# Optimization experiments

Hardware: AMD Instinct MI355X
Metric: run time of the kernel (lower is better)

Reference implementation:

```python
import jax, jax.numpy as jnp
import numpy as np

B, S, D = 2, 2048, 1024
H, KH = 16, 4            # query heads, kv heads
DK = D // H              # 64
REP = H // KH            # queries per kv head


def _rope(x):
    # x: (B, h, S, dk); non-interleaved rotate-half RoPE as in source
    dk = x.shape[-1]
    half = dk // 2
    seq = x.shape[2]
    theta = 10000.0 ** (-(jnp.arange(half, dtype=jnp.float32) / half))
    pos = jnp.arange(seq, dtype=jnp.float32)
    freqs = pos[:, None] * theta[None, :]          # (S, half)
    cos = jnp.cos(freqs)[None, None]               # (1,1,S,half)
    sin = jnp.sin(freqs)[None, None]
    x1, x2 = x[..., :half], x[..., half:]
    return jnp.concatenate([x1 * cos - x2 * sin, x2 * cos + x1 * sin], axis=-1)


def setup_inputs() -> dict:
    key = jax.random.key(0)
    ks = jax.random.split(key, 9)
    sd = 1.0 / np.sqrt(D)
    x = jax.random.normal(ks[0], (B, S, D), dtype=jnp.float32)
    # causal mask: 1 where attend allowed, 0 where masked (mask==0 -> -inf)
    mask = jnp.tril(jnp.ones((S, S), dtype=jnp.int32))[None, None]
    Wq = jax.random.normal(ks[1], (D, H * DK), dtype=jnp.float32) * sd
    bq = jnp.zeros((H * DK,), dtype=jnp.float32)
    Wk = jax.random.normal(ks[2], (D, KH * DK), dtype=jnp.float32) * sd
    bk = jnp.zeros((KH * DK,), dtype=jnp.float32)
    Wv = jax.random.normal(ks[3], (D, KH * DK), dtype=jnp.float32) * sd
    bv = jnp.zeros((KH * DK,), dtype=jnp.float32)
    Wo = jax.random.normal(ks[4], (H * DK, D), dtype=jnp.float32) * sd
    bo = jnp.zeros((D,), dtype=jnp.float32)
    return {"x": x, "mask": mask, "Wq": Wq, "bq": bq, "Wk": Wk, "bk": bk,
            "Wv": Wv, "bv": bv, "Wo": Wo, "bo": bo}


def reference(x, mask, Wq, bq, Wk, bk, Wv, bv, Wo, bo):
    b, s, _ = x.shape
    q = (x @ Wq + bq).reshape(b, s, H, DK).transpose(0, 2, 1, 3)   # (B,H,S,DK)
    k = (x @ Wk + bk).reshape(b, s, KH, DK).transpose(0, 2, 1, 3)  # (B,KH,S,DK)
    v = (x @ Wv + bv).reshape(b, s, KH, DK).transpose(0, 2, 1, 3)
    q = _rope(q)
    k = _rope(k)
    k = jnp.repeat(k, REP, axis=1)  # GQA expand: (B,H,S,DK)
    v = jnp.repeat(v, REP, axis=1)
    attn = jnp.einsum('bhqd,bhkd->bhqk', q, k) / np.sqrt(DK).astype(np.float32)
    attn = jnp.where(mask == 0, -jnp.inf, attn)
    score = jax.nn.softmax(attn, axis=-1)
    out = jnp.einsum('bhqk,bhkd->bhqd', score, v)   # (B,H,S,DK)
    out = out.transpose(0, 2, 1, 3).reshape(b, s, H * DK)
    return out @ Wo + bo
```

## Files before the change

kernel.cpp:

```cpp
#include <hip/hip_runtime.h>
#include <math.h>

#define B_   2
#define S_   2048
#define D_   1024
#define H_   16
#define KH_  4
#define DK_  64

using bf16x8 = __attribute__((ext_vector_type(8))) short;
using bf16x4 = __attribute__((ext_vector_type(4))) short;
using f32x4  = __attribute__((ext_vector_type(4))) float;
using f32x2  = __attribute__((ext_vector_type(2))) float;
using u32x4  = __attribute__((ext_vector_type(4))) unsigned int;
using u32x2  = __attribute__((ext_vector_type(2))) unsigned int;

__device__ inline unsigned short f2bf(float f) {
    unsigned u = __float_as_uint(f);
    u += 0x7FFFu + ((u >> 16) & 1u);
    return (unsigned short)(u >> 16);
}
__device__ inline float bf2f(unsigned short u) {
    return __uint_as_float(((unsigned)u) << 16);
}

#ifdef __has_builtin
#if __has_builtin(__builtin_amdgcn_cvt_pk_bf16_f32)
#define PKBF16 1
#endif
#if __has_builtin(__builtin_amdgcn_exp2f)
#define NEXP2 1
#endif
#endif
__device__ inline unsigned pk2bf(float a, float b) {
#ifdef PKBF16
    auto r = __builtin_amdgcn_cvt_pk_bf16_f32(a, b);
    unsigned u; __builtin_memcpy(&u, &r, 4);
    return u;
#else
    return (unsigned)f2bf(a) | ((unsigned)f2bf(b) << 16);
#endif
}
__device__ inline float fexp2(float x) {
#ifdef NEXP2
    return __builtin_amdgcn_exp2f(x);
#else
    return exp2f(x);
#endif
}

#define GL16(gp, lp) __builtin_amdgcn_global_load_lds( \
    (const __attribute__((address_space(1))) unsigned int*)(gp), \
    (__attribute__((address_space(3))) unsigned int*)(lp), 16, 0, 0)

__global__ __launch_bounds__(256) void prep_kernel(
    const float* __restrict__ x,
    const float* __restrict__ Wq, const float* __restrict__ Wk,
    const float* __restrict__ Wv, const float* __restrict__ Wo,
    unsigned short* __restrict__ xb,
    unsigned short* __restrict__ WqkvT,
    unsigned short* __restrict__ WoT,
    float* __restrict__ sct)
{
    __shared__ float T[64][65];
    const int t = threadIdx.x;
    int bx = blockIdx.x;

    if (bx < 2048) {
        const int i = bx * 256 + t;
        f32x4 a = *(const f32x4*)(x + (long)i * 8);
        f32x4 b = *(const f32x4*)(x + (long)i * 8 + 4);
        bf16x8 o;
        o[0] = (short)f2bf(a[0]); o[1] = (short)f2bf(a[1]);
        o[2] = (short)f2bf(a[2]); o[3] = (short)f2bf(a[3]);
        o[4] = (short)f2bf(b[0]); o[5] = (short)f2bf(b[1]);
        o[6] = (short)f2bf(b[2]); o[7] = (short)f2bf(b[3]);
        *(bf16x8*)(xb + (long)i * 8) = o;
        return;
    }
    if (bx >= 2688) {
        const int idx = (bx - 2688) * 256 + t;
        const int s = idx >> 5, d = idx & 31;
        const float theta = exp2f(-(float)d * (13.287712379549449f / 32.0f));
        const float f = (float)s * theta;
        sct[(long)idx * 2]     = cosf(f);
        sct[(long)idx * 2 + 1] = sinf(f);
        return;
    }
    bx -= 2048;
    const float* in; unsigned short* out; int C;
    if (bx < 256)      { in = Wq; out = WqkvT;               C = 1024; }
    else if (bx < 320) { in = Wk; out = WqkvT + 1024 * 1024; C = 256;  bx -= 256; }
    else if (bx < 384) { in = Wv; out = WqkvT + 1280 * 1024; C = 256;  bx -= 320; }
    else               { in = Wo; out = WoT;                 C = 1024; bx -= 384; }
    const int R  = 1024, nr = 16;
    const int r0 = (bx % nr) * 64;
    const int c0 = (bx / nr) * 64;
    {
        const int r  = t >> 2;
        const int cq = (t & 3) * 16;
        const float* src = in + (long)(r0 + r) * C + c0 + cq;
        #pragma unroll
        for (int i = 0; i < 4; ++i) {
            f32x4 v = *(const f32x4*)(src + i * 4);
            T[r][cq + i * 4 + 0] = v[0];
            T[r][cq + i * 4 + 1] = v[1];
            T[r][cq + i * 4 + 2] = v[2];
            T[r][cq + i * 4 + 3] = v[3];
        }
    }
    __syncthreads();
    {
        const int c  = t >> 2;
        const int rq = (t & 3) * 16;
        bf16x8 p0, p1;
        #pragma unroll
        for (int i = 0; i < 8; ++i) {
            p0[i] = (short)f2bf(T[rq + i][c]);
            p1[i] = (short)f2bf(T[rq + 8 + i][c]);
        }
        unsigned short* dst = out + (long)(c0 + c) * R + r0 + rq;
        *(bf16x8*)dst       = p0;
        *(bf16x8*)(dst + 8) = p1;
    }
}

template<bool BF16OUT>
__global__ __launch_bounds__(256) void gemm64_kernel(
    const unsigned short* __restrict__ A,
    const unsigned short* __restrict__ Bt,
    const float* __restrict__ b0,
    const float* __restrict__ b1,
    const float* __restrict__ b2,
    float* __restrict__ outf,
    unsigned short* __restrict__ outb,
    unsigned short* __restrict__ qbuf,
    unsigned short* __restrict__ kbuf,
    const float* __restrict__ sct,
    int N, int K)
{
    __shared__ unsigned short As[2][64][64];
    __shared__ unsigned short Bs[2][128][64];

    const int t  = threadIdx.x;
    const int m0 = blockIdx.x * 64;
    const int n0 = blockIdx.y * 128;

    const int w    = t >> 6;
    const int lane = t & 63;
    const int n    = lane & 15;
    const int quad = lane >> 4;
    const int wm   = (w >> 1) * 32;
    const int wn   = (w & 1) * 64;

    const int sr8 = lane >> 3;
    const int gch = (lane & 7) ^ sr8;

    const unsigned short* gA = A  + (long)(m0 + w * 8 + sr8) * K + gch * 8;
    const unsigned short* gB = Bt + (long)(n0 + w * 8 + sr8) * K + gch * 8;

    #define STAGE(buf, kk)                                              \
    do {                                                                \
        GL16(gA + (kk),              &As[buf][w * 8][0]);               \
        GL16(gA + 32 * K + (kk),     &As[buf][w * 8 + 32][0]);          \
        GL16(gB + (kk),              &Bs[buf][w * 8][0]);               \
        GL16(gB + 32 * K + (kk),     &Bs[buf][w * 8 + 32][0]);          \
        GL16(gB + 64 * K + (kk),     &Bs[buf][w * 8 + 64][0]);          \
        GL16(gB + 96 * K + (kk),     &Bs[buf][w * 8 + 96][0]);          \
    } while (0)

    STAGE(0, 0);

    f32x4 acc[2][4];
    #pragma unroll
    for (int i = 0; i < 2; ++i)
        #pragma unroll
        for (int j = 0; j < 4; ++j) acc[i][j] = 0.0f;

    const int n7 = n & 7;

    for (int k0 = 0; k0 < K; k0 += 64) {
        const int cur = (k0 >> 6) & 1;
        __syncthreads();
        if (k0 + 64 < K) STAGE(cur ^ 1, k0 + 64);

        #pragma unroll
        for (int kp = 0; kp < 2; ++kp) {
            const int ca = ((kp * 4 + quad) ^ n7) * 8;
            bf16x8 af[2], bfr[4];
            #pragma unroll
            for (int i = 0; i < 2; ++i)
                af[i] = *(const bf16x8*)&As[cur][wm + i * 16 + n][ca];
            #pragma unroll
            for (int j = 0; j < 4; ++j)
                bfr[j] = *(const bf16x8*)&Bs[cur][wn + j * 16 + n][ca];
            #pragma unroll
            for (int mi = 0; mi < 2; ++mi)
                #pragma unroll
                for (int ni = 0; ni < 4; ++ni)
                    acc[mi][ni] = __builtin_amdgcn_mfma_f32_16x16x32_bf16(
                        af[mi], bfr[ni], acc[mi][ni], 0, 0, 0);
        }
    }
    #undef STAGE

    if (BF16OUT) {
        const int colbase = n0 + wn;
        if (colbase < 1280) {
            const bool isQ = colbase < 1024;
            const float scl = isQ ? 0.1803368801111606f : 1.0f;
            const int hh = isQ ? (colbase >> 6) : ((colbase - 1024) >> 6);
            const int HH = isQ ? H_ : KH_;
            unsigned short* obase = isQ ? qbuf : kbuf;
            const int gn0 = colbase + n;
            const float bA = isQ ? b0[gn0]      : b1[gn0 - 1024];
            const float bB = isQ ? b0[gn0 + 16] : b1[gn0 - 1008];
            const float bC = isQ ? b0[gn0 + 32] : b1[gn0 - 992];
            const float bD = isQ ? b0[gn0 + 48] : b1[gn0 - 976];
            #pragma unroll
            for (int mi = 0; mi < 2; ++mi) {
                #pragma unroll
                for (int r = 0; r < 4; ++r) {
                    const int gm = m0 + wm + mi * 16 + quad * 4 + r;
                    const int bb = gm >> 11, s = gm & (S_ - 1);
                    const f32x2 t0 = *(const f32x2*)(sct + ((long)s * 32 + n) * 2);
                    const f32x2 t1 = *(const f32x2*)(sct + ((long)s * 32 + 16 + n) * 2);
                    const float c0 = t0[0] * scl, s0v = t0[1] * scl;
                    const float c1 = t1[0] * scl, s1v = t1[1] * scl;
                    const float x1 = acc[mi][0][r] + bA;
                    const float y1 = acc[mi][1][r] + bB;
                    const float x2 = acc[mi][2][r] + bC;
                    const float y2 = acc[mi][3][r] + bD;
                    unsigned short* dst =
                        obase + ((long)(bb * HH + hh) * S_ + s) * DK_;
                    dst[n]      = f2bf(x1 * c0 - x2 * s0v);
                    dst[16 + n] = f2bf(y1 * c1 - y2 * s1v);
                    dst[32 + n] = f2bf(x2 * c0 + x1 * s0v);
                    dst[48 + n] = f2bf(y2 * c1 + y1 * s1v);
                }
            }
        } else {
            const int hv = (colbase - 1280) >> 6;
            #pragma unroll
            for (int mi = 0; mi < 2; ++mi) {
                const int gm0 = m0 + wm + mi * 16 + quad * 4;
                const int bb  = gm0 >> 11;
                const int s0v = gm0 & (S_ - 1);
                #pragma unroll
                for (int ni = 0; ni < 4; ++ni) {
                    const int d = ni * 16 + n;
                    const float bias = b2[(colbase - 1280) + d];
                    bf16x4 o;
                    o[0] = (short)f2bf(acc[mi][ni][0] + bias);
                    o[1] = (short)f2bf(acc[mi][ni][1] + bias);
                    o[2] = (short)f2bf(acc[mi][ni][2] + bias);
                    o[3] = (short)f2bf(acc[mi][ni][3] + bias);
                    unsigned short* dst = outb +
                        ((long)((bb * KH_ + hv) * DK_ + d)) * S_ + s0v;
                    *(bf16x4*)dst = o;
                }
            }
        }
    } else {
        #pragma unroll
        for (int mi = 0; mi < 2; ++mi) {
            #pragma unroll
            for (int r = 0; r < 4; ++r) {
                const int gm = m0 + wm + mi * 16 + quad * 4 + r;
                #pragma unroll
                for (int ni = 0; ni < 4; ++ni) {
                    const int gn = n0 + wn + ni * 16 + n;
                    outf[(long)gm * N + gn] = acc[mi][ni][r] + b0[gn];
                }
            }
        }
    }
}

__global__ __launch_bounds__(512) void attn_kernel(
    const unsigned short* __restrict__ qb,
    const unsigned short* __restrict__ kbf,
    const unsigned short* __restrict__ vT,
    unsigned short* __restrict__ ot)
{
    __shared__ __align__(16) unsigned short Ks[2][64][64];
    __shared__ __align__(16) unsigned short Vs[2][64][64];
    __shared__ __align__(16) unsigned short Ps[8][16][64];

    const int tid = threadIdx.x;
    const int bx  = blockIdx.x;

    const int j  = bx >> 8;
    const int p  = bx & 255;
    const int g  = p >> 5;
    const int bh = p & 31;
    const int a  = j ? g : (15 - g);

    const int b   = bh >> 4, h = bh & 15;
    const int kh  = h >> 2;
    const int q0  = a * 128;

    const int wv   = tid >> 6;
    const int lane = tid & 63;
    const int n    = lane & 15;
    const int quad = lane >> 4;
    const int xk   = n & 7;

    const unsigned short* qp =
        qb + ((long)(b * H_ + h) * S_ + q0 + wv * 16 + n) * DK_;
    const bf16x8 qa0 = *(const bf16x8*)(qp + quad * 8);
    const bf16x8 qa1 = *(const bf16x8*)(qp + 32 + quad * 8);

    f32x4 O[4];
    #pragma unroll
    for (int dt = 0; dt < 4; ++dt) O[dt] = 0.0f;
    float lsum = 0.f;

    const unsigned short* kbase = kbf + (long)(b * KH_ + kh) * S_ * DK_;
    const unsigned short* vbase = vT  + (long)(b * KH_ + kh) * DK_ * S_;

    const int ntiles = 2 * a + 2;
    const int ub     = 2 * a + (wv >> 2);
    const int srow = tid >> 3;
    const int lc   = tid & 7;
    const int sc8  = lc * 8;
    const int rk   = srow & 7;
    const int pcs  = (lc ^ rk) * 8;

    const int vb0  = (lc & 1) * 16 + ((lc >> 1) & 1) * 4 + (lc >> 2) * 32;
    const int vc1  = vb0 >> 3;
    const int voff = vb0 & 7;
    const int vp1  = ((vc1 ^ rk) * 8) + voff;
    const int vp2  = (((vc1 + 1) ^ rk) * 8) + voff;

    u32x4 kr = *(const u32x4*)(kbase + (long)srow * DK_ + sc8);
    u32x4 vr = *(const u32x4*)(vbase + (long)srow * S_ + sc8);
    *(u32x4*)&Ks[0][srow][pcs] = kr;
    {
        u32x2 va, vb2;
        va[0] = vr[0];  va[1] = vr[1];
        vb2[0] = vr[2]; vb2[1] = vr[3];
        *(u32x2*)&Vs[0][srow][vp1] = va;
        *(u32x2*)&Vs[0][srow][vp2] = vb2;
    }

    for (int u = 0; u < ntiles; ++u) {
        const int cur = u & 1;
        const int kb  = u * 64;
        __syncthreads();

        if (u + 1 < ntiles) {
            const int kbn = kb + 64;
            kr = *(const u32x4*)(kbase + (long)(kbn + srow) * DK_ + sc8);
            vr = *(const u32x4*)(vbase + (long)srow * S_ + kbn + sc8);
        }

        if (u <= ub) {
            f32x4 sc[4];
            #pragma unroll
            for (int ct = 0; ct < 4; ++ct) {
                const bf16x8 kf0 =
                    *(const bf16x8*)&Ks[cur][ct * 16 + n][(quad ^ xk) * 8];
                const bf16x8 kf1 =
                    *(const bf16x8*)&Ks[cur][ct * 16 + n][((quad + 4) ^ xk) * 8];
                f32x4 c = 0.0f;
                c = __builtin_amdgcn_mfma_f32_16x16x32_bf16(kf0, qa0, c, 0, 0, 0);
                c = __builtin_amdgcn_mfma_f32_16x16x32_bf16(kf1, qa1, c, 0, 0, 0);
                sc[ct] = c;
            }

            if (u == ub) {
                const int qg = q0 + wv * 16 + n;
                #pragma unroll
                for (int ct = 0; ct < 4; ++ct) {
                    const int kq = kb + ct * 16 + quad * 4;
                    #pragma unroll
                    for (int r = 0; r < 4; ++r)
                        if (kq + r > qg) sc[ct][r] = -INFINITY;
                }
            }

            f32x4 rs4 = 0.0f;
            #pragma unroll
            for (int ct = 0; ct < 4; ++ct) {
                #pragma unroll
                for (int r = 0; r < 4; ++r) {
                    const float p2 = fexp2(sc[ct][r]);
                    sc[ct][r] = p2;
                    rs4[r] += p2;
                }
            }
            lsum += (rs4[0] + rs4[1]) + (rs4[2] + rs4[3]);

            u32x4 pw0, pw1;
            pw0[0] = pk2bf(sc[0][0], sc[0][1]);
            pw0[1] = pk2bf(sc[0][2], sc[0][3]);
            pw0[2] = pk2bf(sc[1][0], sc[1][1]);
            pw0[3] = pk2bf(sc[1][2], sc[1][3]);
            pw1[0] = pk2bf(sc[2][0], sc[2][1]);
            pw1[1] = pk2bf(sc[2][2], sc[2][3]);
            pw1[2] = pk2bf(sc[3][0], sc[3][1]);
            pw1[3] = pk2bf(sc[3][2], sc[3][3]);
            bf16x8 pb0, pb1;
            __builtin_memcpy(&pb0, &pw0, 16);
            __builtin_memcpy(&pb1, &pw1, 16);

            #pragma unroll
            for (int dt = 0; dt < 4; ++dt) {
                const bf16x8 av0 =
                    *(const bf16x8*)&Vs[cur][dt * 16 + n][(quad ^ xk) * 8];
                const bf16x8 av1 =
                    *(const bf16x8*)&Vs[cur][dt * 16 + n][((quad + 4) ^ xk) * 8];
                O[dt] = __builtin_amdgcn_mfma_f32_16x16x32_bf16(av0, pb0, O[dt], 0, 0, 0);
                O[dt] = __builtin_amdgcn_mfma_f32_16x16x32_bf16(av1, pb1, O[dt], 0, 0, 0);
            }
        }

        if (u + 1 < ntiles) {
            const int nb = cur ^ 1;
            *(u32x4*)&Ks[nb][srow][pcs] = kr;
            u32x2 va, vb2;
            va[0] = vr[0];  va[1] = vr[1];
            vb2[0] = vr[2]; vb2[1] = vr[3];
            *(u32x2*)&Vs[nb][srow][vp1] = va;
            *(u32x2*)&Vs[nb][srow][vp2] = vb2;
        }
    }

    lsum += __shfl_xor(lsum, 16);
    lsum += __shfl_xor(lsum, 32);
    const float inv = 1.0f / lsum;
    #pragma unroll
    for (int dt = 0; dt < 4; ++dt) {
        u32x2 pw;
        pw[0] = pk2bf(O[dt][0] * inv, O[dt][1] * inv);
        pw[1] = pk2bf(O[dt][2] * inv, O[dt][3] * inv);
        const int pc = ((2 * dt + (quad >> 1)) ^ xk) * 8 + (quad & 1) * 4;
        *(u32x2*)&Ps[wv][n][pc] = pw;
    }
    __builtin_amdgcn_s_waitcnt(0);
    const int fr = lane >> 3;
    const int c8l = lane & 7;
    #pragma unroll
    for (int it = 0; it < 2; ++it) {
        const int row = it * 8 + fr;
        const int q   = q0 + wv * 16 + row;
        unsigned short* op = ot + ((long)(b * S_ + q) * H_ + h) * DK_ + c8l * 8;
        *(bf16x8*)op = *(const bf16x8*)&Ps[wv][row][(c8l ^ fr) * 8];
    }
}

extern "C" void kernel_launch(void* const* d_in, const int* in_sizes, int n_in,
                              void* d_out, int out_size, void* d_ws, size_t ws_size,
                              hipStream_t stream)
{
    const float* x  = (const float*)d_in[0];
    const float* Wq = (const float*)d_in[2];
    const float* bq = (const float*)d_in[3];
    const float* Wk = (const float*)d_in[4];
    const float* bk = (const float*)d_in[5];
    const float* Wv = (const float*)d_in[6];
    const float* bv = (const float*)d_in[7];
    const float* Wo = (const float*)d_in[8];
    const float* bo = (const float*)d_in[9];
    float* out = (float*)d_out;

    unsigned short* ws    = (unsigned short*)d_ws;
    unsigned short* xb    = ws;
    unsigned short* qkvm  = xb + 4194304;
    unsigned short* qbuf  = qkvm + 6291456;
    unsigned short* kbuf  = qbuf + 4194304;
    unsigned short* vbuf  = kbuf + 1048576;
    unsigned short* WqkvT = vbuf + 1048576;
    unsigned short* WoT   = WqkvT + 1572864;
    float*          sct   = (float*)(WoT + 1048576);
    unsigned short* ob    = qkvm;

    prep_kernel<<<2944, 256, 0, stream>>>(x, Wq, Wk, Wv, Wo, xb, WqkvT, WoT, sct);

    gemm64_kernel<true><<<dim3(64, 12), 256, 0, stream>>>(
        xb, WqkvT, bq, bk, bv, nullptr, vbuf, qbuf, kbuf, sct, 1536, 1024);

    attn_kernel<<<512, 512, 0, stream>>>(qbuf, kbuf, vbuf, ob);

    gemm64_kernel<false><<<dim3(64, 8), 256, 0, stream>>>(
        ob, WoT, bo, nullptr, nullptr, out, nullptr, nullptr, nullptr, nullptr,
        1024, 1024);
}
```

Before: 163.0 us.

## Widen attention KV tile to 128 keys with per-wave causal skipping

The attention loop now stages 128 keys per iteration instead of 64, which halves the number of K/V tile loads, barriers and loop iterations. On the final diagonal tile, each wave computes only the 16-key sub-blocks its queries can attend to and sets the rest to -inf. The launch bounds also request 4 blocks per CU. The cost is double the K/V shared memory and more live registers for the 8 score tiles, so the occupancy hint may force register spills.

After: 166.9 us. 1.02x slower.

```diff
diff --git a/kernel.cpp b/kernel.cpp
--- a/kernel.cpp
+++ b/kernel.cpp
@@ -277,14 +277,14 @@
     }
 }
 
-__global__ __launch_bounds__(512) void attn_kernel(
+__global__ __launch_bounds__(512, 4) void attn_kernel(
     const unsigned short* __restrict__ qb,
     const unsigned short* __restrict__ kbf,
     const unsigned short* __restrict__ vT,
     unsigned short* __restrict__ ot)
 {
-    __shared__ __align__(16) unsigned short Ks[2][64][64];
-    __shared__ __align__(16) unsigned short Vs[2][64][64];
+    __shared__ __align__(16) unsigned short Ks[2][128][64];
+    __shared__ __align__(16) unsigned short Vs[2][64][128];
     __shared__ __align__(16) unsigned short Ps[8][16][64];
 
     const int tid = threadIdx.x;
@@ -319,8 +319,7 @@
     const unsigned short* kbase = kbf + (long)(b * KH_ + kh) * S_ * DK_;
     const unsigned short* vbase = vT  + (long)(b * KH_ + kh) * DK_ * S_;
 
-    const int ntiles = 2 * a + 2;
-    const int ub     = 2 * a + (wv >> 2);
+    const int ntiles = a + 1;
     const int srow = tid >> 3;
     const int lc   = tid & 7;
     const int sc8  = lc * 8;
@@ -333,32 +332,44 @@
     const int vp1  = ((vc1 ^ rk) * 8) + voff;
     const int vp2  = (((vc1 + 1) ^ rk) * 8) + voff;
 
-    u32x4 kr = *(const u32x4*)(kbase + (long)srow * DK_ + sc8);
-    u32x4 vr = *(const u32x4*)(vbase + (long)srow * S_ + sc8);
-    *(u32x4*)&Ks[0][srow][pcs] = kr;
+    u32x4 kr0 = *(const u32x4*)(kbase + (long)srow * DK_ + sc8);
+    u32x4 kr1 = *(const u32x4*)(kbase + (long)(64 + srow) * DK_ + sc8);
+    u32x4 vr0 = *(const u32x4*)(vbase + (long)srow * S_ + sc8);
+    u32x4 vr1 = *(const u32x4*)(vbase + (long)srow * S_ + 64 + sc8);
     {
-        u32x2 va, vb2;
-        va[0] = vr[0];  va[1] = vr[1];
-        vb2[0] = vr[2]; vb2[1] = vr[3];
-        *(u32x2*)&Vs[0][srow][vp1] = va;
-        *(u32x2*)&Vs[0][srow][vp2] = vb2;
+        *(u32x4*)&Ks[0][srow][pcs]      = kr0;
+        *(u32x4*)&Ks[0][64 + srow][pcs] = kr1;
+        u32x2 h0, h1;
+        h0[0] = vr0[0]; h0[1] = vr0[1];
+        h1[0] = vr0[2]; h1[1] = vr0[3];
+        *(u32x2*)&Vs[0][srow][vp1] = h0;
+        *(u32x2*)&Vs[0][srow][vp2] = h1;
+        h0[0] = vr1[0]; h0[1] = vr1[1];
+        h1[0] = vr1[2]; h1[1] = vr1[3];
+        *(u32x2*)&Vs[0][srow][vp1 + 64] = h0;
+        *(u32x2*)&Vs[0][srow][vp2 + 64] = h1;
     }
 
     for (int u = 0; u < ntiles; ++u) {
         const int cur = u & 1;
-        const int kb  = u * 64;
+        const int kb  = u * 128;
+        const bool last = (u + 1 == ntiles);
         __syncthreads();
 
-        if (u + 1 < ntiles) {
-            const int kbn = kb + 64;
-            kr = *(const u32x4*)(kbase + (long)(kbn + srow) * DK_ + sc8);
-            vr = *(const u32x4*)(vbase + (long)srow * S_ + kbn + sc8);
-        }
-
-        if (u <= ub) {
-            f32x4 sc[4];
-            #pragma unroll
-            for (int ct = 0; ct < 4; ++ct) {
+        if (!last) {
+            const int kbn = kb + 128;
+            kr0 = *(const u32x4*)(kbase + (long)(kbn + srow) * DK_ + sc8);
+            kr1 = *(const u32x4*)(kbase + (long)(kbn + 64 + srow) * DK_ + sc8);
+            vr0 = *(const u32x4*)(vbase + (long)srow * S_ + kbn + sc8);
+            vr1 = *(const u32x4*)(vbase + (long)srow * S_ + kbn + 64 + sc8);
+        }
+
+        const int ctmax = last ? wv : 7;
+
+        f32x4 sc[8];
+        #pragma unroll
+        for (int ct = 0; ct < 8; ++ct) {
+            if (ct <= ctmax) {
                 const bf16x8 kf0 =
                     *(const bf16x8*)&Ks[cur][ct * 16 + n][(quad ^ xk) * 8];
                 const bf16x8 kf1 =
@@ -367,63 +378,73 @@
                 c = __builtin_amdgcn_mfma_f32_16x16x32_bf16(kf0, qa0, c, 0, 0, 0);
                 c = __builtin_amdgcn_mfma_f32_16x16x32_bf16(kf1, qa1, c, 0, 0, 0);
                 sc[ct] = c;
-            }
-
-            if (u == ub) {
-                const int qg = q0 + wv * 16 + n;
-                #pragma unroll
-                for (int ct = 0; ct < 4; ++ct) {
+            } else {
+                sc[ct] = -INFINITY;
+            }
+        }
+
+        if (last) {
+            const int qg = q0 + wv * 16 + n;
+            #pragma unroll
+            for (int ct = 0; ct < 8; ++ct) {
+                if (ct <= ctmax) {
                     const int kq = kb + ct * 16 + quad * 4;
                     #pragma unroll
                     for (int r = 0; r < 4; ++r)
                         if (kq + r > qg) sc[ct][r] = -INFINITY;
                 }
             }
-
-            f32x4 rs4 = 0.0f;
-            #pragma unroll
-            for (int ct = 0; ct < 4; ++ct) {
-                #pragma unroll
-                for (int r = 0; r < 4; ++r) {
-                    const float p2 = fexp2(sc[ct][r]);
-                    sc[ct][r] = p2;
-                    rs4[r] += p2;
+        }
+
+        f32x4 rs4 = 0.0f;
+        #pragma unroll
+        for (int ct = 0; ct < 8; ++ct) {
+            #pragma unroll
+            for (int r = 0; r < 4; ++r) {
+                const float p2 = fexp2(sc[ct][r]);
+                sc[ct][r] = p2;
+                rs4[r] += p2;
+            }
+        }
+        lsum += (rs4[0] + rs4[1]) + (rs4[2] + rs4[3]);
+
+        bf16x8 pb[4];
+        #pragma unroll
+        for (int ks = 0; ks < 4; ++ks) {
+            u32x4 pw;
+            pw[0] = pk2bf(sc[2 * ks][0],     sc[2 * ks][1]);
+            pw[1] = pk2bf(sc[2 * ks][2],     sc[2 * ks][3]);
+            pw[2] = pk2bf(sc[2 * ks + 1][0], sc[2 * ks + 1][1]);
+            pw[3] = pk2bf(sc[2 * ks + 1][2], sc[2 * ks + 1][3]);
+            __builtin_memcpy(&pb[ks], &pw, 16);
+        }
+
+        #pragma unroll
+        for (int dt = 0; dt < 4; ++dt) {
+            #pragma unroll
+            for (int ks = 0; ks < 4; ++ks) {
+                if (!last || 2 * ks <= wv) {
+                    const bf16x8 av = *(const bf16x8*)
+                        &Vs[cur][dt * 16 + n][((ks * 4 + quad) ^ xk) * 8];
+                    O[dt] = __builtin_amdgcn_mfma_f32_16x16x32_bf16(
+                        av, pb[ks], O[dt], 0, 0, 0);
                 }
             }
-            lsum += (rs4[0] + rs4[1]) + (rs4[2] + rs4[3]);
-
-            u32x4 pw0, pw1;
-            pw0[0] = pk2bf(sc[0][0], sc[0][1]);
-            pw0[1] = pk2bf(sc[0][2], sc[0][3]);
-            pw0[2] = pk2bf(sc[1][0], sc[1][1]);
-            pw0[3] = pk2bf(sc[1][2], sc[1][3]);
-            pw1[0] = pk2bf(sc[2][0], sc[2][1]);
-            pw1[1] = pk2bf(sc[2][2], sc[2][3]);
-            pw1[2] = pk2bf(sc[3][0], sc[3][1]);
-            pw1[3] = pk2bf(sc[3][2], sc[3][3]);
-            bf16x8 pb0, pb1;
-            __builtin_memcpy(&pb0, &pw0, 16);
-            __builtin_memcpy(&pb1, &pw1, 16);
-
-            #pragma unroll
-            for (int dt = 0; dt < 4; ++dt) {
-                const bf16x8 av0 =
-                    *(const bf16x8*)&Vs[cur][dt * 16 + n][(quad ^ xk) * 8];
-                const bf16x8 av1 =
-                    *(const bf16x8*)&Vs[cur][dt * 16 + n][((quad + 4) ^ xk) * 8];
-                O[dt] = __builtin_amdgcn_mfma_f32_16x16x32_bf16(av0, pb0, O[dt], 0, 0, 0);
-                O[dt] = __builtin_amdgcn_mfma_f32_16x16x32_bf16(av1, pb1, O[dt], 0, 0, 0);
-            }
-        }
-
-        if (u + 1 < ntiles) {
+        }
+
+        if (!last) {
             const int nb = cur ^ 1;
-            *(u32x4*)&Ks[nb][srow][pcs] = kr;
-            u32x2 va, vb2;
-            va[0] = vr[0];  va[1] = vr[1];
-            vb2[0] = vr[2]; vb2[1] = vr[3];
-            *(u32x2*)&Vs[nb][srow][vp1] = va;
-            *(u32x2*)&Vs[nb][srow][vp2] = vb2;
+            *(u32x4*)&Ks[nb][srow][pcs]      = kr0;
+            *(u32x4*)&Ks[nb][64 + srow][pcs] = kr1;
+            u32x2 h0, h1;
+            h0[0] = vr0[0]; h0[1] = vr0[1];
+            h1[0] = vr0[2]; h1[1] = vr0[3];
+            *(u32x2*)&Vs[nb][srow][vp1] = h0;
+            *(u32x2*)&Vs[nb][srow][vp2] = h1;
+            h0[0] = vr1[0]; h0[1] = vr1[1];
+            h1[0] = vr1[2]; h1[1] = vr1[3];
+            *(u32x2*)&Vs[nb][srow][vp1 + 64] = h0;
+            *(u32x2*)&Vs[nb][srow][vp2 + 64] = h1;
         }
     }
 
```
